# Kernel tuning notes

Hardware: AMD Instinct MI355X
Metric: run time of the kernel (lower is better)

## Reference

```python
import jax, jax.numpy as jnp
import numpy as np

B, LQ, LKV, H, NH = 2, 1024, 4096, 1024, 16
HD = H // NH
EPS = 1e-12


def setup_inputs() -> dict:
    key = jax.random.key(0)
    ks = jax.random.split(key, 8)
    s = 0.02
    return {
        "hidden_states": jax.random.normal(ks[0], (B, LQ, H), jnp.float32),
        "encoder_hidden_states": jax.random.normal(ks[1], (B, LKV, H), jnp.float32),
        "encoder_attention_mask": jnp.ones((B, LKV), jnp.int32),
        "q_w": jax.random.normal(ks[2], (H, H), jnp.float32) * s,
        "q_b": jnp.zeros((H,), jnp.float32),
        "k_w": jax.random.normal(ks[3], (H, H), jnp.float32) * s,
        "k_b": jnp.zeros((H,), jnp.float32),
        "v_w": jax.random.normal(ks[4], (H, H), jnp.float32) * s,
        "v_b": jnp.zeros((H,), jnp.float32),
        "o_w": jax.random.normal(ks[5], (H, H), jnp.float32) * s,
        "o_b": jnp.zeros((H,), jnp.float32),
        "ln_w": jnp.ones((H,), jnp.float32),
        "ln_b": jnp.zeros((H,), jnp.float32),
    }


def _split_heads(x, b):
    # [b, L, H] -> [b, nH, L, hd]
    return x.reshape(b, -1, NH, HD).transpose(0, 2, 1, 3)


def reference(hidden_states, encoder_hidden_states, encoder_attention_mask,
              q_w, q_b, k_w, k_b, v_w, v_b, o_w, o_b, ln_w, ln_b):
    b, lq, h = hidden_states.shape
    q = _split_heads(hidden_states @ q_w.T + q_b, b)            # [b,nH,lq,hd]
    k = _split_heads(encoder_hidden_states @ k_w.T + k_b, b)    # [b,nH,lkv,hd]
    v = _split_heads(encoder_hidden_states @ v_w.T + v_b, b)    # [b,nH,lkv,hd]
    scores = jnp.einsum('bhqd,bhkd->bhqk', q, k) / jnp.sqrt(jnp.asarray(HD, q.dtype))
    mask = encoder_attention_mask[:, None, None, :] == 0
    scores = jnp.where(mask, -jnp.inf, scores)
    probs = jax.nn.softmax(scores, axis=-1)
    ctx = jnp.einsum('bhqk,bhkd->bhqd', probs, v)
    ctx = ctx.transpose(0, 2, 1, 3).reshape(b, lq, h)
    attn_out = ctx @ o_w.T + o_b
    y = attn_out + hidden_states
    mu = jnp.mean(y, axis=-1, keepdims=True)
    var = jnp.mean(jnp.square(y - mu), axis=-1, keepdims=True)
    out = (y - mu) * jax.lax.rsqrt(var + EPS) * ln_w + ln_b
    return (out, scores)
```

## Files before the change

kernel.cpp:

```cpp
#include <hip/hip_runtime.h>


typedef __bf16 bf16x8 __attribute__((ext_vector_type(8)));
typedef float f32x4 __attribute__((ext_vector_type(4)));

constexpr int cH = 1024, cNH = 16, cHD = 64, cB = 2, cLQ = 1024, cLKV = 4096;

__device__ __forceinline__ unsigned short f2b(float f) {
    union { float f; unsigned u; } v; v.f = f;
    unsigned u = v.u;
    return (unsigned short)((u + 0x7fffu + ((u >> 16) & 1u)) >> 16);
}

__global__ void cvt_kernel(const float* __restrict__ src, unsigned short* __restrict__ dst, int n4) {
    int i = blockIdx.x * blockDim.x + threadIdx.x;
    int stride = gridDim.x * blockDim.x;
    for (; i < n4; i += stride) {
        float4 f = ((const float4*)src)[i];
        ushort4 o;
        o.x = f2b(f.x); o.y = f2b(f.y); o.z = f2b(f.z); o.w = f2b(f.w);
        ((ushort4*)dst)[i] = o;
    }
}

template<int EPI>
__global__ __launch_bounds__(256) void gemm_bt(
    const unsigned short* __restrict__ A,
    const unsigned short* __restrict__ W,
    const float* __restrict__ bias,
    const float* __restrict__ resid,
    void* __restrict__ Cout)
{
    constexpr int K = 1024, N = 1024;
    __shared__ unsigned short Asm_[128 * 72];
    __shared__ unsigned short Bsm_[128 * 72];
    const int m0 = blockIdx.x * 128, n0 = blockIdx.y * 128;
    const int t = threadIdx.x;
    const int wv = t >> 6, lane = t & 63, quad = lane >> 4, l16 = lane & 15;
    const int wm = (wv & 1) * 64, wn = (wv >> 1) * 64;

    f32x4 acc[4][4];
#pragma unroll
    for (int i = 0; i < 4; i++)
#pragma unroll
        for (int j = 0; j < 4; j++) acc[i][j] = f32x4{0.f, 0.f, 0.f, 0.f};

    for (int k0 = 0; k0 < K; k0 += 64) {
        __syncthreads();
#pragma unroll
        for (int i = 0; i < 4; i++) {
            int idx = t + i * 256;
            int r = idx >> 3, c = idx & 7;
            *(bf16x8*)(&Asm_[r * 72 + c * 8]) = *(const bf16x8*)(&A[(size_t)(m0 + r) * K + k0 + c * 8]);
            *(bf16x8*)(&Bsm_[r * 72 + c * 8]) = *(const bf16x8*)(&W[(size_t)(n0 + r) * K + k0 + c * 8]);
        }
        __syncthreads();
#pragma unroll
        for (int ks = 0; ks < 64; ks += 32) {
            bf16x8 af[4], bfr[4];
#pragma unroll
            for (int i = 0; i < 4; i++)
                af[i] = *(const bf16x8*)(&Asm_[(wm + 16 * i + l16) * 72 + ks + quad * 8]);
#pragma unroll
            for (int j = 0; j < 4; j++)
                bfr[j] = *(const bf16x8*)(&Bsm_[(wn + 16 * j + l16) * 72 + ks + quad * 8]);
#pragma unroll
            for (int i = 0; i < 4; i++)
#pragma unroll
                for (int j = 0; j < 4; j++)
                    acc[i][j] = __builtin_amdgcn_mfma_f32_16x16x32_bf16(af[i], bfr[j], acc[i][j], 0, 0, 0);
        }
    }
#pragma unroll
    for (int i = 0; i < 4; i++) {
#pragma unroll
        for (int j = 0; j < 4; j++) {
            int n = n0 + wn + 16 * j + l16;
            float bv = bias[n];
#pragma unroll
            for (int r = 0; r < 4; r++) {
                int m = m0 + wm + 16 * i + quad * 4 + r;
                float v = acc[i][j][r] + bv;
                if (EPI == 0) {
                    ((unsigned short*)Cout)[(size_t)m * N + n] = f2b(v);
                } else {
                    v += resid[(size_t)m * N + n];
                    ((float*)Cout)[(size_t)m * N + n] = v;
                }
            }
        }
    }
}

__global__ __launch_bounds__(256) void attn_kernel(
    const unsigned short* __restrict__ Qb,
    const unsigned short* __restrict__ Kb,
    const unsigned short* __restrict__ Vb,
    const int* __restrict__ mask,
    float* __restrict__ scores,
    unsigned short* __restrict__ ctx)
{
    __shared__ unsigned short Qs[64 * 72];
    __shared__ unsigned short Ks[64 * 72];
    __shared__ unsigned short Vs[64 * 72];
    __shared__ unsigned short Ps[64 * 72];
    __shared__ int Ms[64];

    const int qt = blockIdx.x, h = blockIdx.y, b = blockIdx.z;
    const int t = threadIdx.x;
    const int wv = t >> 6, lane = t & 63, quad = lane >> 4, l16 = lane & 15;
    const int q0 = qt * 64;

#pragma unroll
    for (int i = 0; i < 2; i++) {
        int idx = t + i * 256;
        int r = idx >> 3, c = idx & 7;
        *(bf16x8*)(&Qs[r * 72 + c * 8]) =
            *(const bf16x8*)(&Qb[(size_t)(b * cLQ + q0 + r) * cH + h * cHD + c * 8]);
    }

    f32x4 cacc[4];
#pragma unroll
    for (int j = 0; j < 4; j++) cacc[j] = f32x4{0.f, 0.f, 0.f, 0.f};
    float rs[4] = {0.f, 0.f, 0.f, 0.f};

    float* srow = scores + (size_t)(b * cNH + h) * cLQ * cLKV;

    for (int kv0 = 0; kv0 < cLKV; kv0 += 64) {
        __syncthreads();
#pragma unroll
        for (int i = 0; i < 2; i++) {
            int idx = t + i * 256;
            int r = idx >> 3, c = idx & 7;
            *(bf16x8*)(&Ks[r * 72 + c * 8]) =
                *(const bf16x8*)(&Kb[(size_t)(b * cLKV + kv0 + r) * cH + h * cHD + c * 8]);
            union { bf16x8 v; unsigned short s[8]; } u;
            u.v = *(const bf16x8*)(&Vb[(size_t)(b * cLKV + kv0 + r) * cH + h * cHD + c * 8]);
#pragma unroll
            for (int j = 0; j < 8; j++)
                Vs[(c * 8 + j) * 72 + r] = u.s[j];
        }
        if (t < 64) Ms[t] = mask[b * cLKV + kv0 + t];
        __syncthreads();

        f32x4 sacc[4];
#pragma unroll
        for (int j = 0; j < 4; j++) sacc[j] = f32x4{0.f, 0.f, 0.f, 0.f};
#pragma unroll
        for (int ks = 0; ks < 64; ks += 32) {
            bf16x8 aq = *(const bf16x8*)(&Qs[(wv * 16 + l16) * 72 + ks + quad * 8]);
#pragma unroll
            for (int nt = 0; nt < 4; nt++) {
                bf16x8 bk = *(const bf16x8*)(&Ks[(nt * 16 + l16) * 72 + ks + quad * 8]);
                sacc[nt] = __builtin_amdgcn_mfma_f32_16x16x32_bf16(aq, bk, sacc[nt], 0, 0, 0);
            }
        }

#pragma unroll
        for (int nt = 0; nt < 4; nt++) {
            int col = nt * 16 + l16;
            bool live = (Ms[col] != 0);
#pragma unroll
            for (int r = 0; r < 4; r++) {
                int qrow = wv * 16 + quad * 4 + r;
                float s = sacc[nt][r] * 0.125f;
                srow[(size_t)(q0 + qrow) * cLKV + kv0 + col] = live ? s : -__builtin_inff();
                float p = live ? __expf(s) : 0.f;
                rs[r] += p;
                Ps[qrow * 72 + col] = f2b(p);
            }
        }
        __syncthreads();

#pragma unroll
        for (int ks = 0; ks < 64; ks += 32) {
            bf16x8 ap = *(const bf16x8*)(&Ps[(wv * 16 + l16) * 72 + ks + quad * 8]);
#pragma unroll
            for (int dt = 0; dt < 4; dt++) {
                bf16x8 bv = *(const bf16x8*)(&Vs[(dt * 16 + l16) * 72 + ks + quad * 8]);
                cacc[dt] = __builtin_amdgcn_mfma_f32_16x16x32_bf16(ap, bv, cacc[dt], 0, 0, 0);
            }
        }
    }

#pragma unroll
    for (int r = 0; r < 4; r++) {
        float v = rs[r];
        v += __shfl_xor(v, 1);
        v += __shfl_xor(v, 2);
        v += __shfl_xor(v, 4);
        v += __shfl_xor(v, 8);
        rs[r] = v;
    }
#pragma unroll
    for (int dt = 0; dt < 4; dt++) {
#pragma unroll
        for (int r = 0; r < 4; r++) {
            int qrow = wv * 16 + quad * 4 + r;
            ctx[(size_t)(b * cLQ + q0 + qrow) * cH + h * cHD + dt * 16 + l16] = f2b(cacc[dt][r] / rs[r]);
        }
    }
}

__global__ __launch_bounds__(256) void ln_kernel(
    const float* __restrict__ y,
    const float* __restrict__ lw,
    const float* __restrict__ lb,
    float* __restrict__ out)
{
    __shared__ float red[8];
    const int row = blockIdx.x, t = threadIdx.x;
    const float* yr = y + (size_t)row * cH;
    float4 v = ((const float4*)yr)[t];
    float s1 = v.x + v.y + v.z + v.w;
    float s2 = v.x * v.x + v.y * v.y + v.z * v.z + v.w * v.w;
#pragma unroll
    for (int o = 1; o < 64; o <<= 1) {
        s1 += __shfl_xor(s1, o);
        s2 += __shfl_xor(s2, o);
    }
    if ((t & 63) == 0) { red[t >> 6] = s1; red[4 + (t >> 6)] = s2; }
    __syncthreads();
    s1 = red[0] + red[1] + red[2] + red[3];
    s2 = red[4] + red[5] + red[6] + red[7];
    float mu = s1 * (1.f / 1024.f);
    float var = s2 * (1.f / 1024.f) - mu * mu;
    float inv = rsqrtf(fmaxf(var, 0.f) + 1e-12f);
    float4 w4 = ((const float4*)lw)[t];
    float4 b4 = ((const float4*)lb)[t];
    float4 o4;
    o4.x = (v.x - mu) * inv * w4.x + b4.x;
    o4.y = (v.y - mu) * inv * w4.y + b4.y;
    o4.z = (v.z - mu) * inv * w4.z + b4.z;
    o4.w = (v.w - mu) * inv * w4.w + b4.w;
    ((float4*)(out + (size_t)row * cH))[t] = o4;
}

extern "C" void kernel_launch(void* const* d_in, const int* in_sizes, int n_in,
                              void* d_out, int out_size, void* d_ws, size_t ws_size,
                              hipStream_t stream) {
    (void)in_sizes; (void)n_in; (void)out_size; (void)ws_size;
    const float* hidden = (const float*)d_in[0];
    const float* enc    = (const float*)d_in[1];
    const int*   mask   = (const int*)d_in[2];
    const float* q_w = (const float*)d_in[3];
    const float* q_b = (const float*)d_in[4];
    const float* k_w = (const float*)d_in[5];
    const float* k_b = (const float*)d_in[6];
    const float* v_w = (const float*)d_in[7];
    const float* v_b = (const float*)d_in[8];
    const float* o_w = (const float*)d_in[9];
    const float* o_b = (const float*)d_in[10];
    const float* lnw = (const float*)d_in[11];
    const float* lnb = (const float*)d_in[12];

    char* ws = (char*)d_ws;
    unsigned short* hid_b = (unsigned short*)(ws);
    unsigned short* enc_b = (unsigned short*)(ws + ((size_t)4  << 20));
    unsigned short* qw_b  = (unsigned short*)(ws + ((size_t)20 << 20));
    unsigned short* kw_b  = (unsigned short*)(ws + ((size_t)22 << 20));
    unsigned short* vw_b  = (unsigned short*)(ws + ((size_t)24 << 20));
    unsigned short* ow_b  = (unsigned short*)(ws + ((size_t)26 << 20));
    unsigned short* Qb    = (unsigned short*)(ws + ((size_t)28 << 20));
    unsigned short* Kb    = (unsigned short*)(ws + ((size_t)32 << 20));
    unsigned short* Vb    = (unsigned short*)(ws + ((size_t)48 << 20));
    unsigned short* ctxb  = (unsigned short*)(ws + ((size_t)64 << 20));
    float*          yb    = (float*)(ws + ((size_t)68 << 20));

    float* out_ln = (float*)d_out;
    float* out_sc = (float*)d_out + (size_t)cB * cLQ * cH;

    cvt_kernel<<<(cB * cLQ * cH / 4 + 255) / 256, 256, 0, stream>>>(hidden, hid_b, cB * cLQ * cH / 4);
    cvt_kernel<<<(cB * cLKV * cH / 4 + 255) / 256, 256, 0, stream>>>(enc, enc_b, cB * cLKV * cH / 4);
    cvt_kernel<<<(cH * cH / 4 + 255) / 256, 256, 0, stream>>>(q_w, qw_b, cH * cH / 4);
    cvt_kernel<<<(cH * cH / 4 + 255) / 256, 256, 0, stream>>>(k_w, kw_b, cH * cH / 4);
    cvt_kernel<<<(cH * cH / 4 + 255) / 256, 256, 0, stream>>>(v_w, vw_b, cH * cH / 4);
    cvt_kernel<<<(cH * cH / 4 + 255) / 256, 256, 0, stream>>>(o_w, ow_b, cH * cH / 4);

    gemm_bt<0><<<dim3(cB * cLQ / 128, 8), 256, 0, stream>>>(hid_b, qw_b, q_b, nullptr, (void*)Qb);
    gemm_bt<0><<<dim3(cB * cLKV / 128, 8), 256, 0, stream>>>(enc_b, kw_b, k_b, nullptr, (void*)Kb);
    gemm_bt<0><<<dim3(cB * cLKV / 128, 8), 256, 0, stream>>>(enc_b, vw_b, v_b, nullptr, (void*)Vb);

    attn_kernel<<<dim3(cLQ / 64, cNH, cB), 256, 0, stream>>>(Qb, Kb, Vb, mask, out_sc, ctxb);

    gemm_bt<1><<<dim3(cB * cLQ / 128, 8), 256, 0, stream>>>(ctxb, ow_b, o_b, hidden, (void*)yb);
    ln_kernel<<<cB * cLQ, 256, 0, stream>>>(yb, lnw, lnb, out_ln);
}
```

Baseline: 901.2 us.

## Use direct global-to-LDS loads, double-buffer attention K/V, pre-transpose V, fuse QKV launch

Global-to-shared copies in the GEMM and attention kernels now use `global_load_lds` DMA. The attention shared tiles drop their padding and use XOR-swizzled layouts instead. A separate kernel transposes V once, so the attention loop no longer scatters V element by element into LDS. The attention loop double-buffers the K, V and mask tiles, removes one barrier, and writes scores with nontemporal stores. The three projection GEMMs are merged into one launch. Risks: the GEMM tiles are unpadded and unswizzled, so LDS bank conflicts may appear, and the transpose adds an extra pass over V.

```diff
diff --git a/kernel.cpp b/kernel.cpp
--- a/kernel.cpp
+++ b/kernel.cpp
@@ -10,6 +10,15 @@
     union { float f; unsigned u; } v; v.f = f;
     unsigned u = v.u;
     return (unsigned short)((u + 0x7fffu + ((u >> 16) & 1u)) >> 16);
+}
+
+__device__ __forceinline__ unsigned short bf16r(float f) {
+    union { __bf16 h; unsigned short u; } v; v.h = (__bf16)f; return v.u;
+}
+
+__device__ __forceinline__ void gload16(const void* g, void* l) {
+    __builtin_amdgcn_global_load_lds((const __attribute__((address_space(1))) void*)g,
+                                     (__attribute__((address_space(3))) void*)l, 16, 0, 0);
 }
 
 __global__ void cvt_kernel(const float* __restrict__ src, unsigned short* __restrict__ dst, int n4) {
@@ -24,20 +33,21 @@
 }
 
 template<int EPI>
-__global__ __launch_bounds__(256) void gemm_bt(
+__device__ __forceinline__ void gemm_core(
     const unsigned short* __restrict__ A,
     const unsigned short* __restrict__ W,
     const float* __restrict__ bias,
     const float* __restrict__ resid,
-    void* __restrict__ Cout)
+    void* __restrict__ Cout,
+    int m0, int n0)
 {
     constexpr int K = 1024, N = 1024;
-    __shared__ unsigned short Asm_[128 * 72];
-    __shared__ unsigned short Bsm_[128 * 72];
-    const int m0 = blockIdx.x * 128, n0 = blockIdx.y * 128;
+    __shared__ unsigned short Asm_[128 * 64];
+    __shared__ unsigned short Bsm_[128 * 64];
     const int t = threadIdx.x;
     const int wv = t >> 6, lane = t & 63, quad = lane >> 4, l16 = lane & 15;
     const int wm = (wv & 1) * 64, wn = (wv >> 1) * 64;
+    const int sr = t >> 3, sc8 = (t & 7) * 8;
 
     f32x4 acc[4][4];
 #pragma unroll
@@ -49,10 +59,9 @@
         __syncthreads();
 #pragma unroll
         for (int i = 0; i < 4; i++) {
-            int idx = t + i * 256;
-            int r = idx >> 3, c = idx & 7;
-            *(bf16x8*)(&Asm_[r * 72 + c * 8]) = *(const bf16x8*)(&A[(size_t)(m0 + r) * K + k0 + c * 8]);
-            *(bf16x8*)(&Bsm_[r * 72 + c * 8]) = *(const bf16x8*)(&W[(size_t)(n0 + r) * K + k0 + c * 8]);
+            int rr = sr + i * 32;
+            gload16(&A[(size_t)(m0 + rr) * K + k0 + sc8], &Asm_[(t + i * 256) * 8]);
+            gload16(&W[(size_t)(n0 + rr) * K + k0 + sc8], &Bsm_[(t + i * 256) * 8]);
         }
         __syncthreads();
 #pragma unroll
@@ -60,10 +69,10 @@
             bf16x8 af[4], bfr[4];
 #pragma unroll
             for (int i = 0; i < 4; i++)
-                af[i] = *(const bf16x8*)(&Asm_[(wm + 16 * i + l16) * 72 + ks + quad * 8]);
+                af[i] = *(const bf16x8*)(&Asm_[(wm + 16 * i + l16) * 64 + ks + quad * 8]);
 #pragma unroll
             for (int j = 0; j < 4; j++)
-                bfr[j] = *(const bf16x8*)(&Bsm_[(wn + 16 * j + l16) * 72 + ks + quad * 8]);
+                bfr[j] = *(const bf16x8*)(&Bsm_[(wn + 16 * j + l16) * 64 + ks + quad * 8]);
 #pragma unroll
             for (int i = 0; i < 4; i++)
 #pragma unroll
@@ -82,7 +91,7 @@
                 int m = m0 + wm + 16 * i + quad * 4 + r;
                 float v = acc[i][j][r] + bv;
                 if (EPI == 0) {
-                    ((unsigned short*)Cout)[(size_t)m * N + n] = f2b(v);
+                    ((unsigned short*)Cout)[(size_t)m * N + n] = bf16r(v);
                 } else {
                     v += resid[(size_t)m * N + n];
                     ((float*)Cout)[(size_t)m * N + n] = v;
@@ -92,32 +101,96 @@
     }
 }
 
+__global__ __launch_bounds__(256) void gemm_qkv(
+    const unsigned short* __restrict__ hid, const unsigned short* __restrict__ enc,
+    const unsigned short* __restrict__ qw, const unsigned short* __restrict__ kw,
+    const unsigned short* __restrict__ vw,
+    const float* __restrict__ qb, const float* __restrict__ kb, const float* __restrict__ vb,
+    unsigned short* __restrict__ Qo, unsigned short* __restrict__ Ko, unsigned short* __restrict__ Vo)
+{
+    const int z = blockIdx.z;
+    const int M = (z == 0) ? cB * cLQ : cB * cLKV;
+    if ((int)blockIdx.x * 128 >= M) return;
+    const unsigned short* A = (z == 0) ? hid : enc;
+    const unsigned short* W = (z == 0) ? qw : (z == 1) ? kw : vw;
+    const float* bias = (z == 0) ? qb : (z == 1) ? kb : vb;
+    unsigned short* C = (z == 0) ? Qo : (z == 1) ? Ko : Vo;
+    gemm_core<0>(A, W, bias, nullptr, (void*)C, blockIdx.x * 128, blockIdx.y * 128);
+}
+
+__global__ __launch_bounds__(256) void gemm_o(
+    const unsigned short* __restrict__ A, const unsigned short* __restrict__ W,
+    const float* __restrict__ bias, const float* __restrict__ resid, float* __restrict__ C)
+{
+    gemm_core<1>(A, W, bias, resid, (void*)C, blockIdx.x * 128, blockIdx.y * 128);
+}
+
+__global__ __launch_bounds__(256) void vtrans_kernel(const unsigned short* __restrict__ Vb,
+                                                     unsigned short* __restrict__ Vt)
+{
+    __shared__ unsigned short T[64 * 64];
+    const int kv0 = blockIdx.x * 64, h = blockIdx.y, b = blockIdx.z;
+    const int t = threadIdx.x;
+    const int r = t >> 3, c = t & 7;
+#pragma unroll
+    for (int i = 0; i < 2; i++) {
+        int rr = r + i * 32;
+        bf16x8 v = *(const bf16x8*)(&Vb[(size_t)(b * cLKV + kv0 + rr) * cH + h * cHD + c * 8]);
+        int ch = c ^ ((rr ^ (rr >> 3)) & 7);
+        *(bf16x8*)(&T[rr * 64 + ch * 8]) = v;
+    }
+    __syncthreads();
+#pragma unroll
+    for (int i = 0; i < 2; i++) {
+        int rd = r + i * 32;
+        union { bf16x8 v; unsigned short s[8]; } u;
+#pragma unroll
+        for (int j = 0; j < 8; j++) {
+            int kv = c * 8 + j;
+            int ch = (rd >> 3) ^ ((kv ^ (kv >> 3)) & 7);
+            u.s[j] = T[kv * 64 + (ch << 3) + (rd & 7)];
+        }
+        *(bf16x8*)(&Vt[((size_t)(b * cNH + h) * cHD + rd) * cLKV + kv0 + c * 8]) = u.v;
+    }
+}
+
 __global__ __launch_bounds__(256) void attn_kernel(
     const unsigned short* __restrict__ Qb,
     const unsigned short* __restrict__ Kb,
-    const unsigned short* __restrict__ Vb,
+    const unsigned short* __restrict__ Vt,
     const int* __restrict__ mask,
     float* __restrict__ scores,
     unsigned short* __restrict__ ctx)
 {
-    __shared__ unsigned short Qs[64 * 72];
-    __shared__ unsigned short Ks[64 * 72];
-    __shared__ unsigned short Vs[64 * 72];
-    __shared__ unsigned short Ps[64 * 72];
-    __shared__ int Ms[64];
+    __shared__ unsigned short Qs[64 * 64];
+    __shared__ unsigned short Ks[2][64 * 64];
+    __shared__ unsigned short Vs[2][64 * 64];
+    __shared__ unsigned short Ps[64 * 64];
+    __shared__ int Ms[2][64];
 
     const int qt = blockIdx.x, h = blockIdx.y, b = blockIdx.z;
     const int t = threadIdx.x;
     const int wv = t >> 6, lane = t & 63, quad = lane >> 4, l16 = lane & 15;
     const int q0 = qt * 64;
+    const int sr = t >> 3, sc = t & 7;
+
+    const unsigned short* Kbase = Kb + (size_t)b * cLKV * cH + h * cHD;
+    const unsigned short* Vbase = Vt + ((size_t)(b * cNH + h) * cHD) * cLKV;
 
 #pragma unroll
     for (int i = 0; i < 2; i++) {
-        int idx = t + i * 256;
-        int r = idx >> 3, c = idx & 7;
-        *(bf16x8*)(&Qs[r * 72 + c * 8]) =
-            *(const bf16x8*)(&Qb[(size_t)(b * cLQ + q0 + r) * cH + h * cHD + c * 8]);
-    }
+        int rr = sr + i * 32;
+        int cc = (sc ^ (rr & 7)) * 8;
+        gload16(&Qb[(size_t)(b * cLQ + q0 + rr) * cH + h * cHD + cc], &Qs[(t + i * 256) * 8]);
+    }
+#pragma unroll
+    for (int i = 0; i < 2; i++) {
+        int rr = sr + i * 32;
+        int cc = (sc ^ (rr & 7)) * 8;
+        gload16(&Kbase[(size_t)rr * cH + cc], &Ks[0][(t + i * 256) * 8]);
+        gload16(&Vbase[(size_t)rr * cLKV + cc], &Vs[0][(t + i * 256) * 8]);
+    }
+    if (t < 64) Ms[0][t] = mask[b * cLKV + t];
 
     f32x4 cacc[4];
 #pragma unroll
@@ -125,59 +198,62 @@
     float rs[4] = {0.f, 0.f, 0.f, 0.f};
 
     float* srow = scores + (size_t)(b * cNH + h) * cLQ * cLKV;
-
-    for (int kv0 = 0; kv0 < cLKV; kv0 += 64) {
+    const int qr = wv * 16 + l16;
+
+    for (int it = 0; it < cLKV / 64; ++it) {
+        const int kv0 = it * 64, cur = it & 1;
         __syncthreads();
-#pragma unroll
-        for (int i = 0; i < 2; i++) {
-            int idx = t + i * 256;
-            int r = idx >> 3, c = idx & 7;
-            *(bf16x8*)(&Ks[r * 72 + c * 8]) =
-                *(const bf16x8*)(&Kb[(size_t)(b * cLKV + kv0 + r) * cH + h * cHD + c * 8]);
-            union { bf16x8 v; unsigned short s[8]; } u;
-            u.v = *(const bf16x8*)(&Vb[(size_t)(b * cLKV + kv0 + r) * cH + h * cHD + c * 8]);
-#pragma unroll
-            for (int j = 0; j < 8; j++)
-                Vs[(c * 8 + j) * 72 + r] = u.s[j];
-        }
-        if (t < 64) Ms[t] = mask[b * cLKV + kv0 + t];
-        __syncthreads();
+        if (it + 1 < cLKV / 64) {
+            const int kv1 = kv0 + 64;
+#pragma unroll
+            for (int i = 0; i < 2; i++) {
+                int rr = sr + i * 32;
+                int cc = (sc ^ (rr & 7)) * 8;
+                gload16(&Kbase[(size_t)(kv1 + rr) * cH + cc], &Ks[cur ^ 1][(t + i * 256) * 8]);
+                gload16(&Vbase[(size_t)rr * cLKV + kv1 + cc], &Vs[cur ^ 1][(t + i * 256) * 8]);
+            }
+            if (t < 64) Ms[cur ^ 1][t] = mask[b * cLKV + kv1 + t];
+        }
 
         f32x4 sacc[4];
 #pragma unroll
         for (int j = 0; j < 4; j++) sacc[j] = f32x4{0.f, 0.f, 0.f, 0.f};
 #pragma unroll
         for (int ks = 0; ks < 64; ks += 32) {
-            bf16x8 aq = *(const bf16x8*)(&Qs[(wv * 16 + l16) * 72 + ks + quad * 8]);
+            const int ec = (ks >> 3) + quad;
+            bf16x8 aq = *(const bf16x8*)(&Qs[qr * 64 + ((ec ^ (qr & 7)) << 3)]);
 #pragma unroll
             for (int nt = 0; nt < 4; nt++) {
-                bf16x8 bk = *(const bf16x8*)(&Ks[(nt * 16 + l16) * 72 + ks + quad * 8]);
+                int kr = nt * 16 + l16;
+                bf16x8 bk = *(const bf16x8*)(&Ks[cur][kr * 64 + ((ec ^ (kr & 7)) << 3)]);
                 sacc[nt] = __builtin_amdgcn_mfma_f32_16x16x32_bf16(aq, bk, sacc[nt], 0, 0, 0);
             }
         }
 
 #pragma unroll
         for (int nt = 0; nt < 4; nt++) {
-            int col = nt * 16 + l16;
-            bool live = (Ms[col] != 0);
-#pragma unroll
-            for (int r = 0; r < 4; r++) {
-                int qrow = wv * 16 + quad * 4 + r;
-                float s = sacc[nt][r] * 0.125f;
-                srow[(size_t)(q0 + qrow) * cLKV + kv0 + col] = live ? s : -__builtin_inff();
+            const int col = nt * 16 + l16;
+            const bool live = (Ms[cur][col] != 0);
+#pragma unroll
+            for (int r4 = 0; r4 < 4; r4++) {
+                const int qrow = wv * 16 + quad * 4 + r4;
+                float s = sacc[nt][r4] * 0.125f;
+                float sv = live ? s : -__builtin_inff();
+                __builtin_nontemporal_store(sv, &srow[(size_t)(q0 + qrow) * cLKV + kv0 + col]);
                 float p = live ? __expf(s) : 0.f;
-                rs[r] += p;
-                Ps[qrow * 72 + col] = f2b(p);
-            }
-        }
-        __syncthreads();
+                rs[r4] += p;
+                Ps[qrow * 64 + ((((col >> 3) ^ (qrow & 7)) << 3) | (col & 7))] = bf16r(p);
+            }
+        }
 
 #pragma unroll
         for (int ks = 0; ks < 64; ks += 32) {
-            bf16x8 ap = *(const bf16x8*)(&Ps[(wv * 16 + l16) * 72 + ks + quad * 8]);
+            const int ec = (ks >> 3) + quad;
+            bf16x8 ap = *(const bf16x8*)(&Ps[qr * 64 + ((ec ^ (qr & 7)) << 3)]);
 #pragma unroll
             for (int dt = 0; dt < 4; dt++) {
-                bf16x8 bv = *(const bf16x8*)(&Vs[(dt * 16 + l16) * 72 + ks + quad * 8]);
+                int dr = dt * 16 + l16;
+                bf16x8 bv = *(const bf16x8*)(&Vs[cur][dr * 64 + ((ec ^ (dr & 7)) << 3)]);
                 cacc[dt] = __builtin_amdgcn_mfma_f32_16x16x32_bf16(ap, bv, cacc[dt], 0, 0, 0);
             }
         }
@@ -197,7 +273,7 @@
 #pragma unroll
         for (int r = 0; r < 4; r++) {
             int qrow = wv * 16 + quad * 4 + r;
-            ctx[(size_t)(b * cLQ + q0 + qrow) * cH + h * cHD + dt * 16 + l16] = f2b(cacc[dt][r] / rs[r]);
+            ctx[(size_t)(b * cLQ + q0 + qrow) * cH + h * cHD + dt * 16 + l16] = bf16r(cacc[dt][r] / rs[r]);
         }
     }
 }
@@ -266,6 +342,7 @@
     unsigned short* Vb    = (unsigned short*)(ws + ((size_t)48 << 20));
     unsigned short* ctxb  = (unsigned short*)(ws + ((size_t)64 << 20));
     float*          yb    = (float*)(ws + ((size_t)68 << 20));
+    unsigned short* Vt    = (unsigned short*)(ws + ((size_t)76 << 20));
 
     float* out_ln = (float*)d_out;
     float* out_sc = (float*)d_out + (size_t)cB * cLQ * cH;
@@ -277,12 +354,12 @@
     cvt_kernel<<<(cH * cH / 4 + 255) / 256, 256, 0, stream>>>(v_w, vw_b, cH * cH / 4);
     cvt_kernel<<<(cH * cH / 4 + 255) / 256, 256, 0, stream>>>(o_w, ow_b, cH * cH / 4);
 
-    gemm_bt<0><<<dim3(cB * cLQ / 128, 8), 256, 0, stream>>>(hid_b, qw_b, q_b, nullptr, (void*)Qb);
-    gemm_bt<0><<<dim3(cB * cLKV / 128, 8), 256, 0, stream>>>(enc_b, kw_b, k_b, nullptr, (void*)Kb);
-    gemm_bt<0><<<dim3(cB * cLKV / 128, 8), 256, 0, stream>>>(enc_b, vw_b, v_b, nullptr, (void*)Vb);
-
-    attn_kernel<<<dim3(cLQ / 64, cNH, cB), 256, 0, stream>>>(Qb, Kb, Vb, mask, out_sc, ctxb);
-
-    gemm_bt<1><<<dim3(cB * cLQ / 128, 8), 256, 0, stream>>>(ctxb, ow_b, o_b, hidden, (void*)yb);
+    gemm_qkv<<<dim3(64, 8, 3), 256, 0, stream>>>(hid_b, enc_b, qw_b, kw_b, vw_b,
+                                                 q_b, k_b, v_b, Qb, Kb, Vb);
+    vtrans_kernel<<<dim3(cLKV / 64, cNH, cB), 256, 0, stream>>>(Vb, Vt);
+
+    attn_kernel<<<dim3(cLQ / 64, cNH, cB), 256, 0, stream>>>(Qb, Kb, Vt, mask, out_sc, ctxb);
+
+    gemm_o<<<dim3(cB * cLQ / 128, 8), 256, 0, stream>>>(ctxb, ow_b, o_b, hidden, yb);
     ln_kernel<<<cB * cLQ, 256, 0, stream>>>(yb, lnw, lnb, out_ln);
 }
```

Measured after the change: 853.0 us. -5.3%, faster.
